# Kernel optimization log

Hardware: AMD Instinct MI355X
Metric: run time of the kernel (lower is better)

Reference implementation:

```python
import jax, jax.numpy as jnp
import numpy as np

N_NODES = 20000
N_EDGES = 150000
IN_C = 512
OUT_C = 512
K_INIT = 7  # weight has K_INIT+1 = 8 slices, all used by the forward loop


def setup_inputs() -> dict:
    key = jax.random.key(0)
    k1, k2, k3, k4 = jax.random.split(key, 4)
    x = jax.random.normal(k1, (N_NODES, IN_C), dtype=jnp.float32)
    edge_index = jax.random.randint(k2, (2, N_EDGES), 0, N_NODES, dtype=jnp.int32)
    # uniform init as in reset_parameters: bound = 1/sqrt(in_channels * (K+1))
    bound = 1.0 / np.sqrt(IN_C * (K_INIT + 1))
    weight = jax.random.uniform(k3, (K_INIT + 1, IN_C, OUT_C), dtype=jnp.float32,
                                minval=-bound, maxval=bound)
    bias = jax.random.uniform(k4, (OUT_C,), dtype=jnp.float32,
                              minval=-bound, maxval=bound)
    return {"x": x, "edge_index": edge_index, "weight": weight, "bias": bias}


def _spmm(row, col, lap, x, num_nodes):
    # out[i] = sum_{e: row[e]==i} lap[e] * x[col[e]]
    msgs = lap[:, None] * x[col]  # [E, C] gather + scale
    return jax.ops.segment_sum(msgs, row, num_segments=num_nodes)


def reference(x, edge_index, weight, bias):
    row, col = edge_index[0], edge_index[1]
    num_nodes = x.shape[0]
    Kw = weight.shape[0]
    # degree^{-1/2} normalization of implicit adjacency, edge_attr = ones
    deg = jax.ops.segment_sum(jnp.ones_like(row, dtype=x.dtype), row,
                              num_segments=num_nodes)
    dinv = jnp.where(deg > 0, jax.lax.rsqrt(jnp.maximum(deg, 1e-30)), 0.0)
    lap = -dinv[row] * dinv[col]  # [E]
    Tx_0 = x
    out = Tx_0 @ weight[0]
    Tx_1 = _spmm(row, col, lap, x, num_nodes)
    out = out + Tx_1 @ weight[1]
    for k in range(2, Kw):
        Tx_2 = 2.0 * _spmm(row, col, lap, Tx_1, num_nodes) - Tx_0
        out = out + Tx_2 @ weight[k]
        Tx_0, Tx_1 = Tx_1, Tx_2
    return out + bias
```

## Files before the change

### kernel.cpp

```cpp
#include <hip/hip_runtime.h>

#define NN 20000
#define NP 20096
#define NE 150000
#define CC 512
#define KW 8
#define KT 4096
#define SCB 20

typedef __attribute__((ext_vector_type(8))) short short8;
typedef __attribute__((ext_vector_type(4))) float f32x4;
typedef __attribute__((ext_vector_type(8))) unsigned short ushort8v;

__device__ inline unsigned short f2bf(float f) {
  unsigned u = __builtin_bit_cast(unsigned, f);
  u += 0x7fffu + ((u >> 16) & 1u);
  return (unsigned short)(u >> 16);
}

__device__ inline float bf2f(unsigned short u) {
  return __builtin_bit_cast(float, (unsigned)u << 16);
}

__device__ inline void gload_lds16(const void* g, void* l) {
  __builtin_amdgcn_global_load_lds(
      (const __attribute__((address_space(1))) unsigned int*)g,
      (__attribute__((address_space(3))) unsigned int*)l, 16, 0, 0);
}


__global__ __launch_bounds__(256) void k_count(const int* __restrict__ row, int* __restrict__ deg) {
  int e = blockIdx.x * blockDim.x + threadIdx.x;
  if (e < NE) atomicAdd(&deg[row[e]], 1);
}

__global__ __launch_bounds__(1024) void k_scanA(const int* __restrict__ deg,
    int* __restrict__ row_off, int* __restrict__ bsum, float* __restrict__ dinv) {
  __shared__ int sm[1024];
  const int b = blockIdx.x, tid = threadIdx.x;
  int i = b * 1024 + tid;
  int v = (i < NN) ? deg[i] : 0;
  if (i < NN) dinv[i] = (v > 0) ? rsqrtf((float)v) : 0.0f;
  sm[tid] = v;
  __syncthreads();
  #pragma unroll
  for (int off = 1; off < 1024; off <<= 1) {
    int t = (tid >= off) ? sm[tid - off] : 0;
    __syncthreads();
    if (tid >= off) sm[tid] += t;
    __syncthreads();
  }
  if (i < NN) row_off[i] = sm[tid] - v;
  if (tid == 1023) bsum[b] = sm[1023];
}

__global__ __launch_bounds__(64) void k_scanB(int* __restrict__ bsum) {
  if (threadIdx.x == 0) {
    int run = 0;
    for (int b = 0; b < SCB; ++b) { int t = bsum[b]; bsum[b] = run; run += t; }
  }
}

__global__ __launch_bounds__(1024) void k_scanC(int* __restrict__ row_off, const int* __restrict__ bsum) {
  int i = blockIdx.x * 1024 + threadIdx.x;
  if (i < NN) row_off[i] += bsum[blockIdx.x];
  if (i == NN - 1) row_off[NN] = NE;
}

__global__ __launch_bounds__(256) void k_fill(const int* __restrict__ row, const int* __restrict__ col,
    const int* __restrict__ row_off, int* __restrict__ cursor, const float* __restrict__ dinv,
    int* __restrict__ csr_col, float* __restrict__ csr_val) {
  int e = blockIdx.x * blockDim.x + threadIdx.x;
  if (e < NE) {
    int r = row[e], c = col[e];
    int pos = row_off[r] + atomicAdd(&cursor[r], 1);
    csr_col[pos] = c;
    csr_val[pos] = -dinv[r] * dinv[c];
  }
}


__global__ __launch_bounds__(256) void k_cast(const float* __restrict__ W, unsigned short* __restrict__ Bt,
                                              const float* __restrict__ x, unsigned short* __restrict__ txall) {
  __shared__ float sm[64][68];
  const int tid = threadIdx.x;
  if (blockIdx.x < 512) {
    const int t = blockIdx.x;
    const int s = t >> 6;
    const int rem = t & 63;
    const int kt0 = (rem >> 3) * 64;
    const int nt0 = (rem & 7) * 64;
    const float* w = W + ((size_t)s << 18);
    #pragma unroll
    for (int i = 0; i < 4; ++i) {
      int f = tid + i * 256;
      int r = f >> 4;
      int c4 = f & 15;
      float4 v = *(const float4*)&w[(size_t)(kt0 + r) * CC + nt0 + c4 * 4];
      sm[r][c4 * 4 + 0] = v.x; sm[r][c4 * 4 + 1] = v.y;
      sm[r][c4 * 4 + 2] = v.z; sm[r][c4 * 4 + 3] = v.w;
    }
    __syncthreads();
    #pragma unroll
    for (int i = 0; i < 2; ++i) {
      int g = tid + i * 256;
      int nl = g >> 3;
      int k8 = (g & 7) * 8;
      ushort8v o;
      #pragma unroll
      for (int j = 0; j < 8; ++j) o[j] = f2bf(sm[k8 + j][nl]);
      *(ushort8v*)&Bt[(size_t)(nt0 + nl) * KT + s * CC + kt0 + k8] = o;
    }
  } else {
    size_t t = (size_t)(blockIdx.x - 512) * 256 + tid;
    size_t idx = t * 8;
    if (idx >= (size_t)NN * CC) return;
    size_t r = idx >> 9;
    int c = (int)(idx & 511);
    const float4* p = (const float4*)&x[idx];
    float4 a = p[0], b = p[1];
    ushort8v v;
    v[0] = f2bf(a.x); v[1] = f2bf(a.y); v[2] = f2bf(a.z); v[3] = f2bf(a.w);
    v[4] = f2bf(b.x); v[5] = f2bf(b.y); v[6] = f2bf(b.z); v[7] = f2bf(b.w);
    *(ushort8v*)&txall[r * KT + c] = v;
  }
}


__global__ __launch_bounds__(256) void k_spmm(const unsigned short* __restrict__ gsrc,
    const unsigned short* __restrict__ gprev, unsigned short* __restrict__ gdst,
    const int* __restrict__ row_off, const int* __restrict__ csr_col,
    const float* __restrict__ csr_val, float alpha, float beta)
{
  const int tid = threadIdx.x;
  const int i = blockIdx.x * 4 + (tid >> 6);
  const int c8 = (tid & 63) * 8;
  const int e0 = row_off[i];
  const int e1 = row_off[i + 1];
  const int deg = e1 - e0;

  ushort8v pv = {};
  if (beta != 0.0f) pv = *(const ushort8v*)&gprev[(size_t)i * KT + c8];

  float acc[8] = {};
  if (deg <= 0) {
  } else if (deg <= 8) {
    int idxs[8]; float vals[8];
    #pragma unroll
    for (int q = 0; q < 8; ++q) {
      int ee = e0 + q;
      bool ok = ee < e1;
      int ec = ok ? ee : (e1 - 1);
      idxs[q] = csr_col[ec];
      vals[q] = ok ? csr_val[ec] : 0.0f;
    }
    ushort8v xs[8];
    #pragma unroll
    for (int q = 0; q < 8; ++q)
      xs[q] = *(const ushort8v*)&gsrc[(size_t)idxs[q] * KT + c8];
    #pragma unroll
    for (int q = 0; q < 8; ++q)
      #pragma unroll
      for (int p = 0; p < 8; ++p)
        acc[p] += vals[q] * bf2f(xs[q][p]);
  } else if (deg <= 16) {
    int idxs[16]; float vals[16];
    #pragma unroll
    for (int q = 0; q < 16; ++q) {
      int ee = e0 + q;
      bool ok = ee < e1;
      int ec = ok ? ee : (e1 - 1);
      idxs[q] = csr_col[ec];
      vals[q] = ok ? csr_val[ec] : 0.0f;
    }
    ushort8v xs[16];
    #pragma unroll
    for (int q = 0; q < 16; ++q)
      xs[q] = *(const ushort8v*)&gsrc[(size_t)idxs[q] * KT + c8];
    #pragma unroll
    for (int q = 0; q < 16; ++q)
      #pragma unroll
      for (int p = 0; p < 8; ++p)
        acc[p] += vals[q] * bf2f(xs[q][p]);
  } else {
    for (int base = e0; base < e1; base += 8) {
      int idxs[8]; float vals[8];
      #pragma unroll
      for (int q = 0; q < 8; ++q) {
        int ee = base + q;
        bool ok = ee < e1;
        int ec = ok ? ee : (e1 - 1);
        idxs[q] = csr_col[ec];
        vals[q] = ok ? csr_val[ec] : 0.0f;
      }
      ushort8v xs[8];
      #pragma unroll
      for (int q = 0; q < 8; ++q)
        xs[q] = *(const ushort8v*)&gsrc[(size_t)idxs[q] * KT + c8];
      #pragma unroll
      for (int q = 0; q < 8; ++q)
        #pragma unroll
        for (int p = 0; p < 8; ++p)
          acc[p] += vals[q] * bf2f(xs[q][p]);
    }
  }

  ushort8v bv;
  if (beta != 0.0f) {
    #pragma unroll
    for (int q = 0; q < 8; ++q)
      bv[q] = f2bf(alpha * acc[q] + beta * bf2f(pv[q]));
  } else {
    #pragma unroll
    for (int q = 0; q < 8; ++q)
      bv[q] = f2bf(alpha * acc[q]);
  }
  *(ushort8v*)&gdst[(size_t)i * KT + c8] = bv;
}


__global__ __launch_bounds__(256) void k_gemm(const unsigned short* __restrict__ A,
    const unsigned short* __restrict__ Bt, float* __restrict__ C,
    const float* __restrict__ bias)
{
  __shared__ unsigned short smA[128 * 32];
  __shared__ unsigned short smB[128 * 32];
  const int tid  = threadIdx.x;
  const int lane = tid & 63;
  const int wave = tid >> 6;
  const int wr = wave >> 1, wc = wave & 1;

  const int nwg = (NP / 128) * 4;
  int bid = blockIdx.x;
  int q = nwg >> 3, rr = nwg & 7;
  int xcd = bid & 7, lid = bid >> 3;
  int wgid = (xcd < rr ? xcd * (q + 1) : rr * (q + 1) + (xcd - rr) * q) + lid;
  const int m0 = (wgid >> 2) * 128;
  const int n0 = (wgid & 3) * 128;

  const int srow = lane >> 2;
  const int skc  = (lane & 3) * 8;

  f32x4 acc[4][4] = {};

  for (int k0 = 0; k0 < KT; k0 += 32) {
    #pragma unroll
    for (int i = 0; i < 2; ++i) {
      int row = wave * 32 + i * 16;
      gload_lds16(&A[(size_t)(m0 + row + srow) * KT + k0 + skc], &smA[row * 32]);
      gload_lds16(&Bt[(size_t)(n0 + row + srow) * KT + k0 + skc], &smB[row * 32]);
    }
    __syncthreads();

    short8 af[4], bfv[4];
    #pragma unroll
    for (int f = 0; f < 4; ++f) {
      af[f]  = *(const short8*)&smA[(wr * 64 + f * 16 + (lane & 15)) * 32 + (lane >> 4) * 8];
      bfv[f] = *(const short8*)&smB[(wc * 64 + f * 16 + (lane & 15)) * 32 + (lane >> 4) * 8];
    }
    #pragma unroll
    for (int fm = 0; fm < 4; ++fm)
      #pragma unroll
      for (int fn = 0; fn < 4; ++fn)
        acc[fm][fn] = __builtin_amdgcn_mfma_f32_16x16x32_bf16(af[fm], bfv[fn], acc[fm][fn], 0, 0, 0);
    __syncthreads();
  }

  const int prow = (lane >> 4) * 4;
  const int pcol = lane & 15;
  #pragma unroll
  for (int fm = 0; fm < 4; ++fm) {
    #pragma unroll
    for (int fn = 0; fn < 4; ++fn) {
      int gcol = n0 + wc * 64 + fn * 16 + pcol;
      float bb = bias[gcol];
      #pragma unroll
      for (int j = 0; j < 4; ++j) {
        int grow = m0 + wr * 64 + fm * 16 + prow + j;
        if (grow < NN) C[(size_t)grow * CC + gcol] = acc[fm][fn][j] + bb;
      }
    }
  }
}


extern "C" void kernel_launch(void* const* d_in, const int* in_sizes, int n_in,
                              void* d_out, int out_size, void* d_ws, size_t ws_size,
                              hipStream_t stream) {
  const float* x      = (const float*)d_in[0];
  const int*   row    = (const int*)d_in[1];
  const int*   col    = row + NE;
  const float* weight = (const float*)d_in[2];
  const float* bias   = (const float*)d_in[3];
  float* out = (float*)d_out;

  unsigned short* TxAll = (unsigned short*)d_ws;
  unsigned short* Bt    = TxAll + (size_t)NP * KT;
  float* dinv    = (float*)(Bt + (size_t)CC * KT);
  float* csr_val = dinv + NN;
  int*   deg     = (int*)(csr_val + NE);
  int*   cursor  = deg + NN;
  int*   row_off = cursor + NN;
  int*   csr_col = row_off + NN + 1;
  int*   bsum    = csr_col + NE;

  hipMemsetAsync(deg, 0, (size_t)2 * NN * sizeof(int), stream);
  k_count<<<(NE + 255) / 256, 256, 0, stream>>>(row, deg);
  k_scanA<<<SCB, 1024, 0, stream>>>(deg, row_off, bsum, dinv);
  k_scanB<<<1, 64, 0, stream>>>(bsum);
  k_scanC<<<SCB, 1024, 0, stream>>>(row_off, bsum);
  k_fill<<<(NE + 255) / 256, 256, 0, stream>>>(row, col, row_off, cursor, dinv, csr_col, csr_val);

  k_cast<<<512 + (NN * CC / 8 + 255) / 256, 256, 0, stream>>>(weight, Bt, x, TxAll);

  const int spmm_grid = NN / 4;
  k_spmm<<<spmm_grid, 256, 0, stream>>>(TxAll, TxAll, TxAll + CC, row_off, csr_col, csr_val, 1.0f, 0.0f);
  for (int k = 2; k < KW; ++k)
    k_spmm<<<spmm_grid, 256, 0, stream>>>(TxAll + (size_t)(k - 1) * CC, TxAll + (size_t)(k - 2) * CC,
                                          TxAll + (size_t)k * CC, row_off, csr_col, csr_val, 2.0f, -1.0f);

  k_gemm<<<(NP / 128) * 4, 256, 0, stream>>>(TxAll, Bt, out, bias);
}
```

Measured before the change: 336.4 us.

## Use 32x32x16 MFMA in GEMM and merge setup kernels to cut launches

The final GEMM moves from 16x16x32 to 32x32x16 bf16 MFMA tiles with 16-float accumulators, which means fewer LDS fragment loads per MFMA. The scanB kernel is folded into scanC: each block sums the earlier block totals itself. The CSR fill and the weight/x cast kernels are merged into one launch. Together these are meant to cut launch overhead and raise MFMA efficiency, with the risk of LDS bank conflicts under the new fragment access pattern.

```diff
diff --git a/kernel.cpp b/kernel.cpp
--- a/kernel.cpp
+++ b/kernel.cpp
@@ -9,7 +9,7 @@
 #define SCB 20
 
 typedef __attribute__((ext_vector_type(8))) short short8;
-typedef __attribute__((ext_vector_type(4))) float f32x4;
+typedef __attribute__((ext_vector_type(16))) float f32x16;
 typedef __attribute__((ext_vector_type(8))) unsigned short ushort8v;
 
 __device__ inline unsigned short f2bf(float f) {
@@ -54,38 +54,42 @@
   if (tid == 1023) bsum[b] = sm[1023];
 }
 
-__global__ __launch_bounds__(64) void k_scanB(int* __restrict__ bsum) {
+__global__ __launch_bounds__(1024) void k_scanC(int* __restrict__ row_off, const int* __restrict__ bsum) {
+  __shared__ int off;
   if (threadIdx.x == 0) {
-    int run = 0;
-    for (int b = 0; b < SCB; ++b) { int t = bsum[b]; bsum[b] = run; run += t; }
-  }
-}
-
-__global__ __launch_bounds__(1024) void k_scanC(int* __restrict__ row_off, const int* __restrict__ bsum) {
+    int s = 0;
+    for (int j = 0; j < (int)blockIdx.x; ++j) s += bsum[j];
+    off = s;
+  }
+  __syncthreads();
   int i = blockIdx.x * 1024 + threadIdx.x;
-  if (i < NN) row_off[i] += bsum[blockIdx.x];
+  if (i < NN) row_off[i] += off;
   if (i == NN - 1) row_off[NN] = NE;
 }
 
-__global__ __launch_bounds__(256) void k_fill(const int* __restrict__ row, const int* __restrict__ col,
+
+#define FILL_B  ((NE + 255) / 256)
+#define WC_B    512
+#define XC_B    ((NN * CC / 8 + 255) / 256)
+
+__global__ __launch_bounds__(256) void k_fillcast(const int* __restrict__ row, const int* __restrict__ col,
     const int* __restrict__ row_off, int* __restrict__ cursor, const float* __restrict__ dinv,
-    int* __restrict__ csr_col, float* __restrict__ csr_val) {
-  int e = blockIdx.x * blockDim.x + threadIdx.x;
-  if (e < NE) {
-    int r = row[e], c = col[e];
-    int pos = row_off[r] + atomicAdd(&cursor[r], 1);
-    csr_col[pos] = c;
-    csr_val[pos] = -dinv[r] * dinv[c];
-  }
-}
-
-
-__global__ __launch_bounds__(256) void k_cast(const float* __restrict__ W, unsigned short* __restrict__ Bt,
-                                              const float* __restrict__ x, unsigned short* __restrict__ txall) {
+    int* __restrict__ csr_col, float* __restrict__ csr_val,
+    const float* __restrict__ W, unsigned short* __restrict__ Bt,
+    const float* __restrict__ x, unsigned short* __restrict__ txall)
+{
   __shared__ float sm[64][68];
   const int tid = threadIdx.x;
-  if (blockIdx.x < 512) {
-    const int t = blockIdx.x;
+  if (blockIdx.x < FILL_B) {
+    int e = blockIdx.x * 256 + tid;
+    if (e < NE) {
+      int r = row[e], c = col[e];
+      int pos = row_off[r] + atomicAdd(&cursor[r], 1);
+      csr_col[pos] = c;
+      csr_val[pos] = -dinv[r] * dinv[c];
+    }
+  } else if (blockIdx.x < FILL_B + WC_B) {
+    const int t = blockIdx.x - FILL_B;
     const int s = t >> 6;
     const int rem = t & 63;
     const int kt0 = (rem >> 3) * 64;
@@ -112,7 +116,7 @@
       *(ushort8v*)&Bt[(size_t)(nt0 + nl) * KT + s * CC + kt0 + k8] = o;
     }
   } else {
-    size_t t = (size_t)(blockIdx.x - 512) * 256 + tid;
+    size_t t = (size_t)(blockIdx.x - FILL_B - WC_B) * 256 + tid;
     size_t idx = t * 8;
     if (idx >= (size_t)NN * CC) return;
     size_t r = idx >> 9;
@@ -240,8 +244,10 @@
 
   const int srow = lane >> 2;
   const int skc  = (lane & 3) * 8;
-
-  f32x4 acc[4][4] = {};
+  const int r32  = lane & 31;
+  const int kh   = (lane >> 5) * 8;
+
+  f32x16 acc[2][2] = {};
 
   for (int k0 = 0; k0 < KT; k0 += 32) {
     #pragma unroll
@@ -252,32 +258,36 @@
     }
     __syncthreads();
 
-    short8 af[4], bfv[4];
-    #pragma unroll
-    for (int f = 0; f < 4; ++f) {
-      af[f]  = *(const short8*)&smA[(wr * 64 + f * 16 + (lane & 15)) * 32 + (lane >> 4) * 8];
-      bfv[f] = *(const short8*)&smB[(wc * 64 + f * 16 + (lane & 15)) * 32 + (lane >> 4) * 8];
-    }
-    #pragma unroll
-    for (int fm = 0; fm < 4; ++fm)
-      #pragma unroll
-      for (int fn = 0; fn < 4; ++fn)
-        acc[fm][fn] = __builtin_amdgcn_mfma_f32_16x16x32_bf16(af[fm], bfv[fn], acc[fm][fn], 0, 0, 0);
-    __syncthreads();
-  }
-
-  const int prow = (lane >> 4) * 4;
-  const int pcol = lane & 15;
+    short8 af[2][2], bfv[2][2];
+    #pragma unroll
+    for (int f = 0; f < 2; ++f)
+      #pragma unroll
+      for (int h = 0; h < 2; ++h) {
+        af[f][h]  = *(const short8*)&smA[(wr * 64 + f * 32 + r32) * 32 + h * 16 + kh];
+        bfv[f][h] = *(const short8*)&smB[(wc * 64 + f * 32 + r32) * 32 + h * 16 + kh];
+      }
+    #pragma unroll
+    for (int fm = 0; fm < 2; ++fm)
+      #pragma unroll
+      for (int fn = 0; fn < 2; ++fn) {
+        acc[fm][fn] = __builtin_amdgcn_mfma_f32_32x32x16_bf16(af[fm][0], bfv[fn][0], acc[fm][fn], 0, 0, 0);
+        acc[fm][fn] = __builtin_amdgcn_mfma_f32_32x32x16_bf16(af[fm][1], bfv[fn][1], acc[fm][fn], 0, 0, 0);
+      }
+    __syncthreads();
+  }
+
+  const int prow4 = 4 * (lane >> 5);
   #pragma unroll
-  for (int fm = 0; fm < 4; ++fm) {
-    #pragma unroll
-    for (int fn = 0; fn < 4; ++fn) {
-      int gcol = n0 + wc * 64 + fn * 16 + pcol;
+  for (int fm = 0; fm < 2; ++fm) {
+    #pragma unroll
+    for (int fn = 0; fn < 2; ++fn) {
+      int gcol = n0 + wc * 64 + fn * 32 + r32;
       float bb = bias[gcol];
       #pragma unroll
-      for (int j = 0; j < 4; ++j) {
-        int grow = m0 + wr * 64 + fm * 16 + prow + j;
-        if (grow < NN) C[(size_t)grow * CC + gcol] = acc[fm][fn][j] + bb;
+      for (int reg = 0; reg < 16; ++reg) {
+        int rloc = (reg & 3) + 8 * (reg >> 2) + prow4;
+        int grow = m0 + wr * 64 + fm * 32 + rloc;
+        if (grow < NN) C[(size_t)grow * CC + gcol] = acc[fm][fn][reg] + bb;
       }
     }
   }
@@ -307,11 +317,9 @@
   hipMemsetAsync(deg, 0, (size_t)2 * NN * sizeof(int), stream);
   k_count<<<(NE + 255) / 256, 256, 0, stream>>>(row, deg);
   k_scanA<<<SCB, 1024, 0, stream>>>(deg, row_off, bsum, dinv);
-  k_scanB<<<1, 64, 0, stream>>>(bsum);
   k_scanC<<<SCB, 1024, 0, stream>>>(row_off, bsum);
-  k_fill<<<(NE + 255) / 256, 256, 0, stream>>>(row, col, row_off, cursor, dinv, csr_col, csr_val);
-
-  k_cast<<<512 + (NN * CC / 8 + 255) / 256, 256, 0, stream>>>(weight, Bt, x, TxAll);
+  k_fillcast<<<FILL_B + WC_B + XC_B, 256, 0, stream>>>(row, col, row_off, cursor, dinv,
+                                                       csr_col, csr_val, weight, Bt, x, TxAll);
 
   const int spmm_grid = NN / 4;
   k_spmm<<<spmm_grid, 256, 0, stream>>>(TxAll, TxAll, TxAll + CC, row_off, csr_col, csr_val, 1.0f, 0.0f);
```

Measured after the change: 359.3 us. +6.8%, slower.
